# Kernel tuning notes

Measured on AMD Instinct MI355X. Metric: run time of the kernel, lower is better.

The kernel has to match this reference:

```python
import jax, jax.numpy as jnp
import numpy as np

SEQ, BATCH, HIDDEN = 2048, 2, 1024
NUM_HEADS, HEAD_DIM = 16, 64
LN_EPS = 1e-6
NEG_INF = -1e10


def setup_inputs() -> dict:
    key = jax.random.key(0)
    k1, k2, k3, k4 = jax.random.split(key, 4)
    inputs_q = jax.random.normal(k1, (SEQ, BATCH, HIDDEN), dtype=jnp.float32)
    # mask convention (TE flax): True / 1 => position is masked out
    mask = jax.random.randint(k2, (BATCH, 1, SEQ, SEQ), 0, 2).astype(bool)
    ln_scale = jnp.ones((HIDDEN,), dtype=jnp.float32)
    ln_bias = jnp.zeros((HIDDEN,), dtype=jnp.float32)
    # fused QKV kernel (embed, 3, num_heads*head_dim); query column pre-scaled
    # at init by 1/sqrt(head_dim) (scaled_query_init=True)
    w_qkv = jax.random.normal(k3, (HIDDEN, 3, NUM_HEADS * HEAD_DIM), dtype=jnp.float32) / np.sqrt(HIDDEN)
    w_qkv = w_qkv.at[:, 0, :].divide(np.sqrt(HEAD_DIM))
    w_out = jax.random.normal(k4, (NUM_HEADS * HEAD_DIM, HIDDEN), dtype=jnp.float32) / np.sqrt(NUM_HEADS * HEAD_DIM)
    return {"inputs_q": inputs_q, "mask": mask, "ln_scale": ln_scale,
            "ln_bias": ln_bias, "w_qkv": w_qkv, "w_out": w_out}


def _layernorm(x, scale, bias):
    mean = jnp.mean(x, axis=-1, keepdims=True)
    var = jnp.mean(jnp.square(x - mean), axis=-1, keepdims=True)
    return (x - mean) * jax.lax.rsqrt(var + LN_EPS) * scale + bias


def reference(inputs_q, mask, ln_scale, ln_bias, w_qkv, w_out):
    s, b, e = inputs_q.shape  # (seq, batch, hidden): transpose_batch_sequence=True
    ln_out = _layernorm(inputs_q, ln_scale, ln_bias)
    # fused QKV projection: (s,b,e) @ (e,3,H*D) -> (s,b,3,H*D)
    qkv = jnp.einsum('sbe,ekf->sbkf', ln_out, w_qkv)
    q, k, v = qkv[:, :, 0, :], qkv[:, :, 1, :], qkv[:, :, 2, :]
    q = q.reshape(s, b, NUM_HEADS, HEAD_DIM)
    k = k.reshape(s, b, NUM_HEADS, HEAD_DIM)
    v = v.reshape(s, b, NUM_HEADS, HEAD_DIM)
    # core attention, transpose_batch_sequence layout (seq, batch, h, d)
    logits = jnp.einsum('qbhd,kbhd->bhqk', q, k)
    logits = jnp.where(mask, jnp.asarray(NEG_INF, logits.dtype), logits)
    attn = jax.nn.softmax(logits, axis=-1)
    ctx = jnp.einsum('bhqk,kbhd->qbhd', attn, v).reshape(s, b, NUM_HEADS * HEAD_DIM)
    out = jnp.einsum('sbf,fe->sbe', ctx, w_out)
    return out
```

## Files before the change

kernel.cpp:

```cpp
#include <hip/hip_runtime.h>

typedef __bf16 bf16;
typedef __attribute__((ext_vector_type(8))) __bf16 bf16x8;
typedef __attribute__((ext_vector_type(4))) __bf16 bf16x4;
typedef __attribute__((ext_vector_type(4))) float f32x4;
typedef unsigned long long u64;

static constexpr int S = 2048, B = 2, H = 1024, NH = 16, HD = 64;
static constexpr int ROWS = S * B;
static constexpr int NQKV = 3 * NH * HD;
static constexpr int KBLK = 64;
static constexpr int NT = S / KBLK;
static constexpr int NTH = NT / 2;
static constexpr int MW = S / 64;
static constexpr float LOG2E = 1.4426950408889634f;
static constexpr int G0_WG = (NQKV / 128) * (ROWS / 128);
static constexpr int PACK_WG = (B * S * S) / (256 * 16);

__device__ __forceinline__ int swz(int row, int col) { return col ^ ((row & 7) << 3); }

__device__ __forceinline__ void g2l16(const bf16* g, bf16* l) {
  __builtin_amdgcn_global_load_lds((const __attribute__((address_space(1))) void*)g,
                                   (__attribute__((address_space(3))) void*)l, 16, 0, 0);
}

__global__ __launch_bounds__(256) void prep_kernel(const float* __restrict__ wqkv,
                                                   const float* __restrict__ wout,
                                                   bf16* __restrict__ dqkv,
                                                   bf16* __restrict__ dout,
                                                   const float* __restrict__ x,
                                                   const float* __restrict__ sc,
                                                   const float* __restrict__ bi,
                                                   bf16* __restrict__ lnout,
                                                   const void* __restrict__ mask,
                                                   u64* __restrict__ bits) {
  __shared__ float shmem[32 * 33];
  const int bid = blockIdx.x;
  const int tid = threadIdx.x;
  if (bid < 4096) {
    const int bx = bid & 127, by = bid >> 7;
    const bool second = bx >= (NQKV / 32);
    const float* src = second ? wout : wqkv;
    bf16* dst = second ? dout : dqkv;
    const int C = second ? H : NQKV;
    const int c0 = (second ? bx - NQKV / 32 : bx) * 32, r0 = by * 32;
    const int xx = tid & 31, yy = tid >> 5;
#pragma unroll
    for (int i = 0; i < 32; i += 8)
      shmem[(yy + i) * 33 + xx] = src[(size_t)(r0 + yy + i) * C + c0 + xx];
    __syncthreads();
#pragma unroll
    for (int i = 0; i < 32; i += 8) {
      const int col = c0 + yy + i;
      const float scale = (!second && col < 1024) ? LOG2E : 1.0f;
      dst[(size_t)col * H + r0 + xx] = (bf16)(shmem[xx * 33 + yy + i] * scale);
    }
  } else if (bid < 8192) {
    const int row = bid - 4096;
    const float4 v = *(const float4*)&x[(size_t)row * H + tid * 4];
    float s = v.x + v.y + v.z + v.w;
#pragma unroll
    for (int m = 1; m < 64; m <<= 1) s += __shfl_xor(s, m);
    float* red1 = shmem;
    float* red2 = shmem + 8;
    const int w = tid >> 6, lane = tid & 63;
    if (lane == 0) red1[w] = s;
    __syncthreads();
    const float mean = (red1[0] + red1[1] + red1[2] + red1[3]) * (1.0f / H);
    const float dx = v.x - mean, dy = v.y - mean, dz = v.z - mean, dw = v.w - mean;
    float q = dx * dx + dy * dy + dz * dz + dw * dw;
#pragma unroll
    for (int m = 1; m < 64; m <<= 1) q += __shfl_xor(q, m);
    if (lane == 0) red2[w] = q;
    __syncthreads();
    const float var = (red2[0] + red2[1] + red2[2] + red2[3]) * (1.0f / H);
    const float inv = rsqrtf(var + 1e-6f);
    const float4 s4 = *(const float4*)&sc[tid * 4];
    const float4 b4 = *(const float4*)&bi[tid * 4];
    bf16x4 o;
    o[0] = (bf16)(dx * inv * s4.x + b4.x);
    o[1] = (bf16)(dy * inv * s4.y + b4.y);
    o[2] = (bf16)(dz * inv * s4.z + b4.z);
    o[3] = (bf16)(dw * inv * s4.w + b4.w);
    *(bf16x4*)&lnout[(size_t)row * H + tid * 4] = o;
  } else {
    const int p = bid - 8192;
    const size_t base = (size_t)p * 4096;
    int* det = (int*)shmem;
    if (tid == 0) det[0] = 0;
    __syncthreads();
    const uint4 wv = *(const uint4*)((const unsigned char*)mask + base + (size_t)tid * 16);
    const unsigned any3 = (wv.x | wv.y | wv.z | wv.w) & 0xFFFFFF00u;
    if (any3) atomicOr(det, 1);
    __syncthreads();
    const bool imode = (det[0] == 0);
#pragma unroll
    for (int k = 0; k < 16; ++k) {
      const size_t e = base + k * 256 + tid;
      int mv;
      if (imode) mv = ((const int*)mask)[e];
      else mv = (int)((const unsigned char*)mask)[e];
      const u64 bal = __ballot(mv != 0);
      if ((tid & 63) == 0) bits[e >> 6] = bal;
    }
  }
}

template <int EPI>
__global__ __launch_bounds__(256) void gemm128(const bf16* __restrict__ A, const bf16* __restrict__ Bt,
                                               bf16* __restrict__ qo, bf16* __restrict__ ko,
                                               bf16* __restrict__ vo, float* __restrict__ out) {
  constexpr int K = 1024;
  constexpr int NKT = K / 64;
  __shared__ __align__(16) bf16 As[2][128][64];
  __shared__ __align__(16) bf16 Bs[2][128][64];
  int lin, NX, total;
  if (EPI == 0) {
    lin = blockIdx.x;
    NX = NQKV / 128; total = G0_WG;
  } else {
    lin = blockIdx.y * gridDim.x + blockIdx.x;
    NX = gridDim.x; total = gridDim.x * gridDim.y;
  }
  const int cpx = total >> 3;
  const int work = (lin & 7) * cpx + (lin >> 3);
  const int bm = (work / NX) * 128, bn = (work % NX) * 128;
  const bool isV = (EPI == 0) && (bn >= 2048);
  const int tid = threadIdx.x;
  const int wave = tid >> 6, lane = tid & 63;
  const int wm = (wave >> 1) * 64, wn = (wave & 1) * 64;
  const int g = lane >> 4, l15 = lane & 15;
  const int lr = lane >> 3;
  const int lc = 8 * ((lane & 7) ^ lr);
  const bf16* Ab = &A[(size_t)bm * K];
  const bf16* Bb = &Bt[(size_t)bn * K];

  f32x4 acc[4][4] = {};
#pragma unroll
  for (int p = 0; p < 4; ++p) {
    const int r0 = wave * 32 + p * 8;
    g2l16(&Ab[(size_t)(r0 + lr) * K + lc], &As[0][r0][0]);
    g2l16(&Bb[(size_t)(r0 + lr) * K + lc], &Bs[0][r0][0]);
  }

  for (int kt = 0; kt < NKT; ++kt) {
    const int cur = kt & 1;
    if (kt + 1 < NKT) {
      const int ko2 = (kt + 1) * 64;
#pragma unroll
      for (int p = 0; p < 4; ++p) {
        const int r0 = wave * 32 + p * 8;
        g2l16(&Ab[(size_t)(r0 + lr) * K + ko2 + lc], &As[cur ^ 1][r0][0]);
        g2l16(&Bb[(size_t)(r0 + lr) * K + ko2 + lc], &Bs[cur ^ 1][r0][0]);
      }
      asm volatile("s_waitcnt vmcnt(8)" ::: "memory");
    } else {
      asm volatile("s_waitcnt vmcnt(0)" ::: "memory");
    }
    __builtin_amdgcn_sched_barrier(0);
    __builtin_amdgcn_s_barrier();
    __builtin_amdgcn_sched_barrier(0);
#pragma unroll
    for (int ks = 0; ks < 2; ++ks) {
      bf16x8 af[4], bb[4];
#pragma unroll
      for (int i = 0; i < 4; ++i) af[i] = *(const bf16x8*)&As[cur][wm + i * 16 + l15][swz(l15, ks * 32 + g * 8)];
#pragma unroll
      for (int j = 0; j < 4; ++j) bb[j] = *(const bf16x8*)&Bs[cur][wn + j * 16 + l15][swz(l15, ks * 32 + g * 8)];
      __builtin_amdgcn_s_setprio(1);
      if (isV) {
#pragma unroll
        for (int i = 0; i < 4; ++i)
#pragma unroll
          for (int j = 0; j < 4; ++j)
            acc[i][j] = __builtin_amdgcn_mfma_f32_16x16x32_bf16(bb[j], af[i], acc[i][j], 0, 0, 0);
      } else {
#pragma unroll
        for (int i = 0; i < 4; ++i)
#pragma unroll
          for (int j = 0; j < 4; ++j)
            acc[i][j] = __builtin_amdgcn_mfma_f32_16x16x32_bf16(af[i], bb[j], acc[i][j], 0, 0, 0);
      }
      __builtin_amdgcn_s_setprio(0);
    }
    __builtin_amdgcn_sched_barrier(0);
    asm volatile("s_waitcnt lgkmcnt(0)" ::: "memory");
    __builtin_amdgcn_sched_barrier(0);
    __builtin_amdgcn_s_barrier();
    __builtin_amdgcn_sched_barrier(0);
  }
#pragma unroll
  for (int i = 0; i < 4; ++i) {
#pragma unroll
    for (int j = 0; j < 4; ++j) {
#pragma unroll
      for (int r = 0; r < 4; ++r) {
        const float val = acc[i][j][r];
        if (isV) {
          const int row = bm + wm + i * 16 + l15;
          const int col = bn + wn + j * 16 + g * 4 + r;
          const int f = col & 1023;
          const int h = f >> 6, d = f & 63;
          const int sdx = row >> 1, b = row & 1;
          vo[(((size_t)b * NH + h) * HD + d) * S + sdx] = (bf16)val;
        } else if (EPI == 0) {
          const int row = bm + wm + i * 16 + g * 4 + r;
          const int col = bn + wn + j * 16 + l15;
          const int kk = col >> 10, f = col & 1023;
          const int h = f >> 6, d = f & 63;
          const int sdx = row >> 1, b = row & 1;
          const size_t head = (size_t)b * NH + h;
          if (kk == 0)
            qo[(head * S + sdx) * HD + d] = (bf16)val;
          else
            ko[(head * S + sdx) * HD + d] = (bf16)val;
        } else {
          const int row = bm + wm + i * 16 + g * 4 + r;
          const int col = bn + wn + j * 16 + l15;
          out[(size_t)row * H + col] = val;
        }
      }
    }
  }
}

__global__ __launch_bounds__(512, 4) void attn_kernel(const bf16* __restrict__ Qb, const bf16* __restrict__ Kb,
                                                      const bf16* __restrict__ Vt, const u64* __restrict__ mbits,
                                                      bf16* __restrict__ p0, bf16* __restrict__ p1,
                                                      float* __restrict__ lsumW) {
  __shared__ __align__(16) bf16 Ks[2][64][64];
  __shared__ __align__(16) bf16 Vs[2][64][64];
  __shared__ __align__(16) bf16 P[8][16][64];
  const int lin = blockIdx.y * 16 + blockIdx.x;
  const int work = ((lin & 7) << 7) | (lin >> 3);
  const int qb = work & 15;
  const int half = (work >> 4) & 1;
  const int bh = work >> 5;
  const int b = bh >> 4, h = bh & 15;
  const int tid = threadIdx.x, w = tid >> 6, lane = tid & 63;
  const int g = lane >> 4, c = lane & 15;
  const int q0 = qb * 128 + w * 16;
  const size_t head = (size_t)b * NH + h;
  const bf16* Qh = Qb + head * S * HD;
  const bf16* Kh = Kb + head * S * HD;
  const bf16* Vh = Vt + head * HD * S;
  const int t0 = half * NTH;

  const int srow = w * 8 + (lane >> 3);
  const int scol = 8 * ((lane & 7) ^ (lane >> 3));

  bf16x8 aq[2];
#pragma unroll
  for (int ks = 0; ks < 2; ++ks)
    aq[ks] = *(const bf16x8*)&Qh[(size_t)(q0 + c) * HD + ks * 32 + g * 8];

  f32x4 o[4] = {};
  float lsum = 0.f;

  g2l16(&Kh[(size_t)(t0 * KBLK + srow) * HD + scol], &Ks[0][w * 8][0]);
  g2l16(&Vh[(size_t)srow * S + t0 * KBLK + scol], &Vs[0][w * 8][0]);
  __syncthreads();

  for (int tt = 0; tt < NTH; ++tt) {
    const int t = t0 + tt;
    const int cur = tt & 1;
    if (tt + 1 < NTH) {
      const int kt1 = (t + 1) * KBLK;
      g2l16(&Kh[(size_t)(kt1 + srow) * HD + scol], &Ks[cur ^ 1][w * 8][0]);
      g2l16(&Vh[(size_t)srow * S + kt1 + scol], &Vs[cur ^ 1][w * 8][0]);
    }
    f32x4 sv[4] = {};
#pragma unroll
    for (int ks = 0; ks < 2; ++ks) {
      bf16x8 bk[4];
#pragma unroll
      for (int j = 0; j < 4; ++j)
        bk[j] = *(const bf16x8*)&Ks[cur][j * 16 + c][swz(c, ks * 32 + g * 8)];
      __builtin_amdgcn_s_setprio(1);
#pragma unroll
      for (int j = 0; j < 4; ++j)
        sv[j] = __builtin_amdgcn_mfma_f32_16x16x32_bf16(bk[j], aq[ks], sv[j], 0, 0, 0);
      __builtin_amdgcn_s_setprio(0);
    }
    {
      const u64 mb = mbits[((size_t)b * S + q0 + c) * MW + t];
      const unsigned mlo = (unsigned)mb, mhi = (unsigned)(mb >> 32);
      f32x4 acc4 = {0.f, 0.f, 0.f, 0.f};
#pragma unroll
      for (int j = 0; j < 4; ++j) {
        const unsigned word = (j < 2) ? mlo : mhi;
        const unsigned sub = word >> (((j & 1) << 4) + (g << 2));
        bf16x4 pk;
#pragma unroll
        for (int r = 0; r < 4; ++r) {
          float e = __builtin_amdgcn_exp2f(sv[j][r]);
          if ((sub >> r) & 1u) e = 0.f;
          pk[r] = (bf16)e;
          acc4[r] += e;
        }
        *(bf16x4*)&P[w][c][(j * 16 + g * 4) ^ ((c & 7) << 3)] = pk;
      }
      lsum += (acc4[0] + acc4[1]) + (acc4[2] + acc4[3]);
    }
    __threadfence_block();
#pragma unroll
    for (int ks = 0; ks < 2; ++ks) {
      const bf16x8 pa = *(const bf16x8*)&P[w][c][(ks * 32 + g * 8) ^ ((c & 7) << 3)];
      bf16x8 bv[4];
#pragma unroll
      for (int j = 0; j < 4; ++j)
        bv[j] = *(const bf16x8*)&Vs[cur][j * 16 + c][swz(c, ks * 32 + g * 8)];
      __builtin_amdgcn_s_setprio(1);
#pragma unroll
      for (int j = 0; j < 4; ++j)
        o[j] = __builtin_amdgcn_mfma_f32_16x16x32_bf16(pa, bv[j], o[j], 0, 0, 0);
      __builtin_amdgcn_s_setprio(0);
    }
    __syncthreads();
  }
  lsum += __shfl_xor(lsum, 16);
  lsum += __shfl_xor(lsum, 32);
  if (lane < 16)
    lsumW[(size_t)half * (B * NH * S) + head * S + q0 + lane] = lsum;
  bf16* dst = half ? p1 : p0;
#pragma unroll
  for (int r = 0; r < 4; ++r) {
    const int qrow = q0 + g * 4 + r;
#pragma unroll
    for (int j = 0; j < 4; ++j)
      dst[((size_t)qrow * B + b) * H + h * HD + j * 16 + c] = (bf16)o[j][r];
  }
}

__global__ __launch_bounds__(256) void combine_kernel(const bf16* __restrict__ p1,
                                                      const float* __restrict__ lsumW,
                                                      bf16* __restrict__ ctx) {
  const int row = blockIdx.x;
  const int col = threadIdx.x * 4;
  const int qrow = row >> 1, b = row & 1;
  const int h = col >> 6;
  const size_t li = (size_t)(b * NH + h) * S + qrow;
  const float l = lsumW[li] + lsumW[(size_t)(B * NH * S) + li];
  const float inv = 1.0f / l;
  const bf16x4 a = *(const bf16x4*)&ctx[(size_t)row * H + col];
  const bf16x4 bb = *(const bf16x4*)&p1[(size_t)row * H + col];
  bf16x4 o;
#pragma unroll
  for (int i = 0; i < 4; ++i) o[i] = (bf16)(((float)a[i] + (float)bb[i]) * inv);
  *(bf16x4*)&ctx[(size_t)row * H + col] = o;
}

extern "C" void kernel_launch(void* const* d_in, const int* in_sizes, int n_in,
                              void* d_out, int out_size, void* d_ws, size_t ws_size,
                              hipStream_t stream) {
  const float* x = (const float*)d_in[0];
  const void* mask = d_in[1];
  const float* ln_scale = (const float*)d_in[2];
  const float* ln_bias = (const float*)d_in[3];
  const float* w_qkv = (const float*)d_in[4];
  const float* w_out = (const float*)d_in[5];
  float* out = (float*)d_out;

  char* ws = (char*)d_ws;
  size_t off = 0;
  u64* mbits = (u64*)(ws + off); off += (size_t)B * S * (S / 8);
  bf16* lnb   = (bf16*)(ws + off); off += (size_t)ROWS * H * 2;
  bf16* wqkvt = (bf16*)(ws + off); off += (size_t)NQKV * H * 2;
  bf16* woutt = (bf16*)(ws + off); off += (size_t)H * H * 2;
  bf16* Qb    = (bf16*)(ws + off); off += (size_t)B * NH * S * HD * 2;
  bf16* Kb    = (bf16*)(ws + off); off += (size_t)B * NH * S * HD * 2;
  bf16* Vt    = (bf16*)(ws + off); off += (size_t)B * NH * S * HD * 2;
  bf16* ctx   = (bf16*)(ws + off); off += (size_t)ROWS * H * 2;

  prep_kernel<<<8192 + PACK_WG, 256, 0, stream>>>(w_qkv, w_out, wqkvt, woutt, x, ln_scale, ln_bias, lnb,
                                                  mask, mbits);
  gemm128<0><<<G0_WG, 256, 0, stream>>>(lnb, wqkvt, Qb, Kb, Vt, nullptr);
  attn_kernel<<<dim3(16, 64), 512, 0, stream>>>(Qb, Kb, Vt, mbits, ctx, lnb, (float*)wqkvt);
  combine_kernel<<<ROWS, 256, 0, stream>>>(lnb, (const float*)wqkvt, ctx);
  gemm128<1><<<dim3(H / 128, ROWS / 128), 256, 0, stream>>>(ctx, woutt, nullptr, nullptr, nullptr, out);
}
```

Measured before the change: 145.4 us.

## Enlarge attention query tile to 32 rows per wave, shrink key block to 32

Each wave now processes 32 query rows (two 16-row tiles) instead of 16, so each K/V tile loaded into LDS is reused across more queries and the grid halves to 512 workgroups. The key block shrinks from 64 to 32, with warps 0-3 staging K and warps 4-7 staging V, and the mask is read as 32-bit words. This cuts LDS and global traffic per query, but doubles the number of loop iterations and barriers, raises register pressure (occupancy hint lowered to 2), and reduces the workgroup count available to fill the CUs.

```diff
diff --git a/kernel.cpp b/kernel.cpp
--- a/kernel.cpp
+++ b/kernel.cpp
@@ -9,10 +9,9 @@
 static constexpr int S = 2048, B = 2, H = 1024, NH = 16, HD = 64;
 static constexpr int ROWS = S * B;
 static constexpr int NQKV = 3 * NH * HD;
-static constexpr int KBLK = 64;
-static constexpr int NT = S / KBLK;
-static constexpr int NTH = NT / 2;
-static constexpr int MW = S / 64;
+static constexpr int KBLK = 32;
+static constexpr int NT32 = S / KBLK;
+static constexpr int NTH = NT32 / 2;
 static constexpr float LOG2E = 1.4426950408889634f;
 static constexpr int G0_WG = (NQKV / 128) * (ROWS / 128);
 static constexpr int PACK_WG = (B * S * S) / (256 * 16);
@@ -224,111 +223,130 @@
   }
 }
 
-__global__ __launch_bounds__(512, 4) void attn_kernel(const bf16* __restrict__ Qb, const bf16* __restrict__ Kb,
+__global__ __launch_bounds__(512, 2) void attn_kernel(const bf16* __restrict__ Qb, const bf16* __restrict__ Kb,
                                                       const bf16* __restrict__ Vt, const u64* __restrict__ mbits,
                                                       bf16* __restrict__ p0, bf16* __restrict__ p1,
                                                       float* __restrict__ lsumW) {
-  __shared__ __align__(16) bf16 Ks[2][64][64];
-  __shared__ __align__(16) bf16 Vs[2][64][64];
-  __shared__ __align__(16) bf16 P[8][16][64];
-  const int lin = blockIdx.y * 16 + blockIdx.x;
-  const int work = ((lin & 7) << 7) | (lin >> 3);
-  const int qb = work & 15;
-  const int half = (work >> 4) & 1;
-  const int bh = work >> 5;
+  __shared__ __align__(16) bf16 Ks[2][32][64];
+  __shared__ __align__(16) bf16 Vs[2][64][32];
+  __shared__ __align__(16) bf16 P[8][2][16][32];
+  const int lin = blockIdx.y * 8 + blockIdx.x;
+  const int work = ((lin & 7) << 6) | (lin >> 3);
+  const int qb = work & 7;
+  const int half = (work >> 3) & 1;
+  const int bh = work >> 4;
   const int b = bh >> 4, h = bh & 15;
   const int tid = threadIdx.x, w = tid >> 6, lane = tid & 63;
   const int g = lane >> 4, c = lane & 15;
-  const int q0 = qb * 128 + w * 16;
+  const int q0 = qb * 256 + w * 32;
   const size_t head = (size_t)b * NH + h;
   const bf16* Qh = Qb + head * S * HD;
   const bf16* Kh = Kb + head * S * HD;
   const bf16* Vh = Vt + head * HD * S;
+  const unsigned* m32 = (const unsigned*)mbits;
   const int t0 = half * NTH;
 
-  const int srow = w * 8 + (lane >> 3);
-  const int scol = 8 * ((lane & 7) ^ (lane >> 3));
-
-  bf16x8 aq[2];
-#pragma unroll
-  for (int ks = 0; ks < 2; ++ks)
-    aq[ks] = *(const bf16x8*)&Qh[(size_t)(q0 + c) * HD + ks * 32 + g * 8];
-
-  f32x4 o[4] = {};
-  float lsum = 0.f;
-
-  g2l16(&Kh[(size_t)(t0 * KBLK + srow) * HD + scol], &Ks[0][w * 8][0]);
-  g2l16(&Vh[(size_t)srow * S + t0 * KBLK + scol], &Vs[0][w * 8][0]);
+  const bool kstage = (w < 4);
+  const int krow = (w & 3) * 8 + (lane >> 3);
+  const int kscol = 8 * ((lane & 7) ^ (lane >> 3));
+  const int vrow = (w & 3) * 16 + (lane >> 2);
+  const int vscol = 8 * ((lane & 3) ^ ((lane >> 2) & 3));
+  bf16* kdst0 = &Ks[0][(w & 3) * 8][0];
+  bf16* kdst1 = &Ks[1][(w & 3) * 8][0];
+  bf16* vdst0 = &Vs[0][(w & 3) * 16][0];
+  bf16* vdst1 = &Vs[1][(w & 3) * 16][0];
+
+  const int bkc0 = swz(c, g * 8);
+  const int bkc1 = swz(c, 32 + g * 8);
+  const int pvc = (g * 8) ^ ((c & 3) << 3);
+
+  bf16x8 aq[2][2];
+#pragma unroll
+  for (int i = 0; i < 2; ++i)
+#pragma unroll
+    for (int ks = 0; ks < 2; ++ks)
+      aq[i][ks] = *(const bf16x8*)&Qh[(size_t)(q0 + i * 16 + c) * HD + ks * 32 + g * 8];
+
+  f32x4 o[2][4] = {};
+  float lsum[2] = {0.f, 0.f};
+
+  if (kstage) g2l16(&Kh[(size_t)(t0 * KBLK + krow) * HD + kscol], kdst0);
+  else        g2l16(&Vh[(size_t)vrow * S + t0 * KBLK + vscol], vdst0);
   __syncthreads();
 
   for (int tt = 0; tt < NTH; ++tt) {
     const int t = t0 + tt;
     const int cur = tt & 1;
     if (tt + 1 < NTH) {
-      const int kt1 = (t + 1) * KBLK;
-      g2l16(&Kh[(size_t)(kt1 + srow) * HD + scol], &Ks[cur ^ 1][w * 8][0]);
-      g2l16(&Vh[(size_t)srow * S + kt1 + scol], &Vs[cur ^ 1][w * 8][0]);
-    }
-    f32x4 sv[4] = {};
+      const int kv1 = (t + 1) * KBLK;
+      if (kstage) g2l16(&Kh[(size_t)(kv1 + krow) * HD + kscol], cur ? kdst0 : kdst1);
+      else        g2l16(&Vh[(size_t)vrow * S + kv1 + vscol], cur ? vdst0 : vdst1);
+    }
+    f32x4 sv[2][2] = {};
 #pragma unroll
     for (int ks = 0; ks < 2; ++ks) {
-      bf16x8 bk[4];
-#pragma unroll
-      for (int j = 0; j < 4; ++j)
-        bk[j] = *(const bf16x8*)&Ks[cur][j * 16 + c][swz(c, ks * 32 + g * 8)];
+      const bf16x8 bk0 = *(const bf16x8*)&Ks[cur][c][ks ? bkc1 : bkc0];
+      const bf16x8 bk1 = *(const bf16x8*)&Ks[cur][16 + c][ks ? bkc1 : bkc0];
       __builtin_amdgcn_s_setprio(1);
 #pragma unroll
-      for (int j = 0; j < 4; ++j)
-        sv[j] = __builtin_amdgcn_mfma_f32_16x16x32_bf16(bk[j], aq[ks], sv[j], 0, 0, 0);
+      for (int i = 0; i < 2; ++i) {
+        sv[i][0] = __builtin_amdgcn_mfma_f32_16x16x32_bf16(bk0, aq[i][ks], sv[i][0], 0, 0, 0);
+        sv[i][1] = __builtin_amdgcn_mfma_f32_16x16x32_bf16(bk1, aq[i][ks], sv[i][1], 0, 0, 0);
+      }
       __builtin_amdgcn_s_setprio(0);
     }
-    {
-      const u64 mb = mbits[((size_t)b * S + q0 + c) * MW + t];
-      const unsigned mlo = (unsigned)mb, mhi = (unsigned)(mb >> 32);
+#pragma unroll
+    for (int i = 0; i < 2; ++i) {
+      const unsigned mw = m32[((size_t)b * S + q0 + i * 16 + c) * 64 + t];
       f32x4 acc4 = {0.f, 0.f, 0.f, 0.f};
 #pragma unroll
-      for (int j = 0; j < 4; ++j) {
-        const unsigned word = (j < 2) ? mlo : mhi;
-        const unsigned sub = word >> (((j & 1) << 4) + (g << 2));
+      for (int j = 0; j < 2; ++j) {
+        const unsigned sub = mw >> (j * 16 + g * 4);
         bf16x4 pk;
 #pragma unroll
         for (int r = 0; r < 4; ++r) {
-          float e = __builtin_amdgcn_exp2f(sv[j][r]);
+          float e = __builtin_amdgcn_exp2f(sv[i][j][r]);
           if ((sub >> r) & 1u) e = 0.f;
           pk[r] = (bf16)e;
           acc4[r] += e;
         }
-        *(bf16x4*)&P[w][c][(j * 16 + g * 4) ^ ((c & 7) << 3)] = pk;
-      }
-      lsum += (acc4[0] + acc4[1]) + (acc4[2] + acc4[3]);
+        *(bf16x4*)&P[w][i][c][(j * 16 + g * 4) ^ ((c & 3) << 3)] = pk;
+      }
+      lsum[i] += (acc4[0] + acc4[1]) + (acc4[2] + acc4[3]);
     }
     __threadfence_block();
-#pragma unroll
-    for (int ks = 0; ks < 2; ++ks) {
-      const bf16x8 pa = *(const bf16x8*)&P[w][c][(ks * 32 + g * 8) ^ ((c & 7) << 3)];
+    {
+      const bf16x8 pa0 = *(const bf16x8*)&P[w][0][c][pvc];
+      const bf16x8 pa1 = *(const bf16x8*)&P[w][1][c][pvc];
       bf16x8 bv[4];
 #pragma unroll
-      for (int j = 0; j < 4; ++j)
-        bv[j] = *(const bf16x8*)&Vs[cur][j * 16 + c][swz(c, ks * 32 + g * 8)];
+      for (int jd = 0; jd < 4; ++jd)
+        bv[jd] = *(const bf16x8*)&Vs[cur][jd * 16 + c][pvc];
       __builtin_amdgcn_s_setprio(1);
 #pragma unroll
-      for (int j = 0; j < 4; ++j)
-        o[j] = __builtin_amdgcn_mfma_f32_16x16x32_bf16(pa, bv[j], o[j], 0, 0, 0);
+      for (int jd = 0; jd < 4; ++jd) {
+        o[0][jd] = __builtin_amdgcn_mfma_f32_16x16x32_bf16(pa0, bv[jd], o[0][jd], 0, 0, 0);
+        o[1][jd] = __builtin_amdgcn_mfma_f32_16x16x32_bf16(pa1, bv[jd], o[1][jd], 0, 0, 0);
+      }
       __builtin_amdgcn_s_setprio(0);
     }
     __syncthreads();
   }
-  lsum += __shfl_xor(lsum, 16);
-  lsum += __shfl_xor(lsum, 32);
-  if (lane < 16)
-    lsumW[(size_t)half * (B * NH * S) + head * S + q0 + lane] = lsum;
   bf16* dst = half ? p1 : p0;
 #pragma unroll
-  for (int r = 0; r < 4; ++r) {
-    const int qrow = q0 + g * 4 + r;
-#pragma unroll
-    for (int j = 0; j < 4; ++j)
-      dst[((size_t)qrow * B + b) * H + h * HD + j * 16 + c] = (bf16)o[j][r];
+  for (int i = 0; i < 2; ++i) {
+    float ls = lsum[i];
+    ls += __shfl_xor(ls, 16);
+    ls += __shfl_xor(ls, 32);
+    if (lane < 16)
+      lsumW[(size_t)half * (B * NH * S) + head * S + q0 + i * 16 + lane] = ls;
+#pragma unroll
+    for (int r = 0; r < 4; ++r) {
+      const int qrow = q0 + i * 16 + g * 4 + r;
+#pragma unroll
+      for (int jd = 0; jd < 4; ++jd)
+        dst[((size_t)qrow * B + b) * H + h * HD + jd * 16 + c] = (bf16)o[i][jd][r];
+    }
   }
 }
 
@@ -375,7 +393,7 @@
   prep_kernel<<<8192 + PACK_WG, 256, 0, stream>>>(w_qkv, w_out, wqkvt, woutt, x, ln_scale, ln_bias, lnb,
                                                   mask, mbits);
   gemm128<0><<<G0_WG, 256, 0, stream>>>(lnb, wqkvt, Qb, Kb, Vt, nullptr);
-  attn_kernel<<<dim3(16, 64), 512, 0, stream>>>(Qb, Kb, Vt, mbits, ctx, lnb, (float*)wqkvt);
+  attn_kernel<<<dim3(8, 64), 512, 0, stream>>>(Qb, Kb, Vt, mbits, ctx, lnb, (float*)wqkvt);
   combine_kernel<<<ROWS, 256, 0, stream>>>(lnb, (const float*)wqkvt, ctx);
   gemm128<1><<<dim3(H / 128, ROWS / 128), 256, 0, stream>>>(ctx, woutt, nullptr, nullptr, nullptr, out);
 }
```

Result: slower. 148.7 us (+2.3%).
